# Performance work log

Hardware: AMD Instinct MI355X
Metric: run time of the kernel (lower is better)

The kernel has to match this reference:

```python
import jax, jax.numpy as jnp
import numpy as np

BERT_DIM = 768
N_ROWS = 5
N_COLS = 12
LN_EPS = 1e-5


def setup_inputs() -> dict:
    key = jax.random.key(0)
    ks = jax.random.split(key, 12)
    B, S = 256, 512
    token_hidden = jax.random.normal(ks[0], (B, S, BERT_DIM), dtype=jnp.float32)
    attention_mask = jax.random.randint(ks[1], (B, S), 0, 2, dtype=jnp.int32)
    s = lambda fan_in: 1.0 / np.sqrt(fan_in)
    return {
        "token_hidden": token_hidden,
        "attention_mask": attention_mask,
        # token_attention: Linear(768,128) -> Tanh -> Linear(128,1)
        "att_w1": jax.random.normal(ks[2], (128, BERT_DIM), dtype=jnp.float32) * s(BERT_DIM),
        "att_b1": jnp.zeros((128,), dtype=jnp.float32),
        "att_w2": jax.random.normal(ks[3], (1, 128), dtype=jnp.float32) * s(128),
        "att_b2": jnp.zeros((1,), dtype=jnp.float32),
        # feature_projector: Linear(768,256) -> GELU -> Dropout(eval) -> Linear(256,5)
        "proj_w1": jax.random.normal(ks[4], (256, BERT_DIM), dtype=jnp.float32) * s(BERT_DIM),
        "proj_b1": jnp.zeros((256,), dtype=jnp.float32),
        "proj_w2": jax.random.normal(ks[5], (N_ROWS, 256), dtype=jnp.float32) * s(256),
        "proj_b2": jnp.zeros((N_ROWS,), dtype=jnp.float32),
        # LayerNorm([5, 12])
        "ln_gamma": jnp.ones((N_ROWS, N_COLS), dtype=jnp.float32),
        "ln_beta": jnp.zeros((N_ROWS, N_COLS), dtype=jnp.float32),
    }


def reference(token_hidden, attention_mask, att_w1, att_b1, att_w2, att_b2,
              proj_w1, proj_b1, proj_w2, proj_b2, ln_gamma, ln_beta):
    # token attention scores: [B, S]
    h = jnp.tanh(jnp.einsum("bsd,hd->bsh", token_hidden, att_w1) + att_b1)
    scores = (jnp.einsum("bsh,oh->bso", h, att_w2) + att_b2)[..., 0]
    scores = jnp.where(attention_mask == 0, jnp.finfo(scores.dtype).min, scores)
    weights = jax.nn.softmax(scores, axis=-1)
    # top-k token selection (indices sorted ascending to preserve order)
    k = min(N_COLS, token_hidden.shape[1])
    _, top_idx = jax.lax.top_k(weights, k)  # [B, k]
    top_idx = jnp.sort(top_idx, axis=-1)
    selected = jnp.take_along_axis(token_hidden, top_idx[:, :, None], axis=1)  # [B, k, D]
    # feature projector (dropout is eval no-op)
    f = jax.nn.gelu(jnp.einsum("bkd,hd->bkh", selected, proj_w1) + proj_b1, approximate=False)
    f = jnp.einsum("bkh,rh->bkr", f, proj_w2) + proj_b2  # [B, k, n_rows]
    features = jnp.transpose(f, (0, 2, 1))  # [B, n_rows, k]
    if features.shape[-1] < N_COLS:
        features = jnp.pad(features, ((0, 0), (0, 0), (0, N_COLS - features.shape[-1])))
    # LayerNorm over trailing [n_rows, n_cols]
    mean = jnp.mean(features, axis=(-2, -1), keepdims=True)
    var = jnp.var(features, axis=(-2, -1), keepdims=True)
    return ln_gamma * (features - mean) * jax.lax.rsqrt(var + LN_EPS) + ln_beta
```

## Files before the change

### kernel.cpp

```cpp
#include <hip/hip_runtime.h>
#include <math.h>

#define B_BATCH 256
#define S_LEN   512
#define D_DIM   768
#define H_ATT   128
#define TOPK    12
#define NCAND   16
#define H_PROJ  256
#define N_ROWS  5
#define N_COLS  12

typedef __bf16 bf16x4 __attribute__((ext_vector_type(4)));
typedef __bf16 bf16x8 __attribute__((ext_vector_type(8)));
typedef float  f32x4  __attribute__((ext_vector_type(4)));

#define WS_SCORES 0
#define WS_WHI    524288
#define WS_WLO    720896
#define WS_W1Q    917504

__global__ __launch_bounds__(256) void prep_kernel(
    const float* __restrict__ w1, __bf16* __restrict__ whi,
    __bf16* __restrict__ wlo, float* __restrict__ w1q)
{
    int id = blockIdx.x * 256 + threadIdx.x;
    if (id < 98304) {
        int j    = id & 7;
        int lane = (id >> 3) & 63;
        int rest = id >> 9;
        int kt   = rest % 24;
        int nt   = rest / 24;
        int n = nt * 16 + (lane & 15);
        int k = kt * 32 + (lane >> 4) * 8 + j;
        float f = w1[n * D_DIM + k];
        __bf16 h = (__bf16)f;
        whi[id] = h;
        wlo[id] = (__bf16)(f - (float)h);
    } else {
        int e2 = id - 98304;
        int i  = e2 & 3;
        int n  = (e2 >> 2) & 127;
        int k4 = e2 >> 9;
        w1q[e2] = w1[n * D_DIM + k4 * 4 + i];
    }
}

__global__ __launch_bounds__(256, 3) void score_mfma(
    const float*  __restrict__ th,
    const __bf16* __restrict__ whi,
    const __bf16* __restrict__ wlo,
    const float*  __restrict__ b1,
    const float*  __restrict__ w2,
    float* __restrict__ scores)
{
    __shared__ __bf16 Ah[8 * 512];
    __shared__ __bf16 Al[8 * 512];
    __shared__ __bf16 Bh[8 * 512];
    __shared__ __bf16 Bl[8 * 512];

    const int tid = threadIdx.x;
    const int wv  = tid >> 6;
    const int ln  = tid & 63;
    const int mblk = blockIdx.x * 128;

    f32x4 acc[2][8];
    const f32x4 z = {0.f, 0.f, 0.f, 0.f};
#pragma unroll
    for (int i = 0; i < 2; ++i)
#pragma unroll
        for (int j = 0; j < 8; ++j) acc[i][j] = z;

    for (int kt = 0; kt < 24; ++kt) {
        float4 v[4];
#pragma unroll
        for (int i = 0; i < 4; ++i) {
            int f = tid + 256 * i;
            int row = f >> 3, q = f & 7;
            v[i] = *(const float4*)(th + (size_t)(mblk + row) * D_DIM + kt * 32 + q * 4);
        }
        uint4 bb[4];
#pragma unroll
        for (int i = 0; i < 4; ++i) {
            int f = tid + 256 * i;
            int r = f & 511;
            int nt = r >> 6, l = r & 63;
            const __bf16* src = (f >> 9) ? wlo : whi;
            bb[i] = *(const uint4*)(src + ((size_t)(nt * 24 + kt) * 64 + l) * 8);
        }
        __syncthreads();

#pragma unroll
        for (int i = 0; i < 4; ++i) {
            int f = tid + 256 * i;
            int row = f >> 3, q = f & 7;
            int mt = row >> 4, kq = q >> 1;
            int l16 = (row & 15) | (kq << 4);
            int a16 = l16 ^ (kq << 2);
            __bf16 h0 = (__bf16)v[i].x, h1 = (__bf16)v[i].y;
            __bf16 h2 = (__bf16)v[i].z, h3 = (__bf16)v[i].w;
            bf16x4 hv = {h0, h1, h2, h3};
            bf16x4 lv = {(__bf16)(v[i].x - (float)h0), (__bf16)(v[i].y - (float)h1),
                         (__bf16)(v[i].z - (float)h2), (__bf16)(v[i].w - (float)h3)};
            int off = mt * 512 + a16 * 8 + (q & 1) * 4;
            *(bf16x4*)(&Ah[off]) = hv;
            *(bf16x4*)(&Al[off]) = lv;
        }
#pragma unroll
        for (int i = 0; i < 4; ++i) {
            int f = tid + 256 * i;
            int r = f & 511;
            int nt = r >> 6, l = r & 63;
            __bf16* dst = (f >> 9) ? Bl : Bh;
            *(uint4*)(&dst[nt * 512 + l * 8]) = bb[i];
        }
        __syncthreads();

        const int al = ln ^ (((ln >> 4) & 3) << 2);
        bf16x8 ah0 = *(bf16x8*)(&Ah[(wv * 2 + 0) * 512 + al * 8]);
        bf16x8 ah1 = *(bf16x8*)(&Ah[(wv * 2 + 1) * 512 + al * 8]);
        bf16x8 al0 = *(bf16x8*)(&Al[(wv * 2 + 0) * 512 + al * 8]);
        bf16x8 al1 = *(bf16x8*)(&Al[(wv * 2 + 1) * 512 + al * 8]);
#pragma unroll
        for (int nt = 0; nt < 8; ++nt) {
            bf16x8 bh = *(bf16x8*)(&Bh[nt * 512 + ln * 8]);
            bf16x8 bl = *(bf16x8*)(&Bl[nt * 512 + ln * 8]);
            acc[0][nt] = __builtin_amdgcn_mfma_f32_16x16x32_bf16(ah0, bh, acc[0][nt], 0, 0, 0);
            acc[0][nt] = __builtin_amdgcn_mfma_f32_16x16x32_bf16(ah0, bl, acc[0][nt], 0, 0, 0);
            acc[0][nt] = __builtin_amdgcn_mfma_f32_16x16x32_bf16(al0, bh, acc[0][nt], 0, 0, 0);
            acc[1][nt] = __builtin_amdgcn_mfma_f32_16x16x32_bf16(ah1, bh, acc[1][nt], 0, 0, 0);
            acc[1][nt] = __builtin_amdgcn_mfma_f32_16x16x32_bf16(ah1, bl, acc[1][nt], 0, 0, 0);
            acc[1][nt] = __builtin_amdgcn_mfma_f32_16x16x32_bf16(al1, bh, acc[1][nt], 0, 0, 0);
        }
    }

    const int col = ln & 15;
    float b1v[8], w2v[8];
#pragma unroll
    for (int nt = 0; nt < 8; ++nt) {
        b1v[nt] = b1[nt * 16 + col];
        w2v[nt] = w2[nt * 16 + col];
    }
#pragma unroll
    for (int mf = 0; mf < 2; ++mf)
#pragma unroll
        for (int r = 0; r < 4; ++r) {
            float s = 0.f;
#pragma unroll
            for (int nt = 0; nt < 8; ++nt)
                s += tanhf(acc[mf][nt][r] + b1v[nt]) * w2v[nt];
            s += __shfl_xor(s, 1, 64);
            s += __shfl_xor(s, 2, 64);
            s += __shfl_xor(s, 4, 64);
            s += __shfl_xor(s, 8, 64);
            if (col == 0)
                scores[mblk + wv * 32 + mf * 16 + (ln >> 4) * 4 + r] = s;
        }
}

__global__ __launch_bounds__(256) void select_kernel(
    const float* __restrict__ th,
    const int*   __restrict__ mask,
    const float* __restrict__ ascores,
    const float* __restrict__ w1q,
    const float* __restrict__ ab1,
    const float* __restrict__ aw2,
    const float* __restrict__ pw1,
    const float* __restrict__ pb1,
    const float* __restrict__ pw2,
    const float* __restrict__ pb2,
    const float* __restrict__ gamma,
    const float* __restrict__ beta,
    float* __restrict__ out)
{
    const int b   = blockIdx.x;
    const int tid = threadIdx.x;
    const int wv  = tid >> 6;
    const int ln  = tid & 63;

    __shared__ float4 xc[NCAND][192];
    __shared__ float sc[S_LEN];
    __shared__ unsigned long long wbest[4];
    __shared__ int   cand[NCAND];
    __shared__ float redW[4][8];
    __shared__ float exact_sc[NCAND];
    __shared__ int   sel_slot[TOPK];
    __shared__ float gbuf[TOPK][H_PROJ + 1];
    __shared__ float feat[N_ROWS * N_COLS];
    __shared__ float stats[2];

    const float NEG_MIN = -3.402823466e38f;

    for (int i = tid; i < S_LEN; i += 256) {
        float s = ascores[(size_t)b * S_LEN + i];
        sc[i] = (mask[(size_t)b * S_LEN + i] == 0) ? NEG_MIN : s;
    }
    __syncthreads();

    for (int it = 0; it < NCAND; ++it) {
        float v0 = sc[tid], v1 = sc[tid + 256];
        unsigned k0 = __float_as_uint(v0);
        k0 = ((int)k0 >= 0) ? (k0 | 0x80000000u) : ~k0;
        unsigned k1 = __float_as_uint(v1);
        k1 = ((int)k1 >= 0) ? (k1 | 0x80000000u) : ~k1;
        unsigned long long p0 = ((unsigned long long)k0 << 32) | (0xFFFFFFFFu - (unsigned)tid);
        unsigned long long p1 = ((unsigned long long)k1 << 32) | (0xFFFFFFFFu - (unsigned)(tid + 256));
        unsigned long long best = p0 > p1 ? p0 : p1;
#pragma unroll
        for (int m = 1; m <= 32; m <<= 1) {
            unsigned long long o = __shfl_xor(best, m, 64);
            if (o > best) best = o;
        }
        if (ln == 0) wbest[wv] = best;
        __syncthreads();
        if (tid == 0) {
            unsigned long long bb = wbest[0];
            for (int w = 1; w < 4; ++w) if (wbest[w] > bb) bb = wbest[w];
            int idx = (int)(0xFFFFFFFFu - (unsigned)(bb & 0xFFFFFFFFu));
            cand[it] = idx;
            sc[idx] = -INFINITY;
        }
        __syncthreads();
    }

#pragma unroll
    for (int i = 0; i < 12; ++i) {
        int f = tid + 256 * i;
        int c = f / 192, k4 = f % 192;
        xc[c][k4] = *(const float4*)(th + ((size_t)b * S_LEN + cand[c]) * D_DIM + k4 * 4);
    }
    __syncthreads();

    {
        const int n = tid & 127;
        const int h = tid >> 7;
        float accs[8];
#pragma unroll
        for (int ci = 0; ci < 8; ++ci) accs[ci] = 0.f;
        for (int k4 = 0; k4 < 192; ++k4) {
            float4 w = *(const float4*)(w1q + (size_t)(k4 * 128 + n) * 4);
#pragma unroll
            for (int ci = 0; ci < 8; ++ci) {
                float4 x = xc[2 * ci + h][k4];
                accs[ci] += w.x * x.x + w.y * x.y + w.z * x.z + w.w * x.w;
            }
        }
        float b1n = ab1[n], w2n = aw2[n];
#pragma unroll
        for (int ci = 0; ci < 8; ++ci) {
            float val = tanhf(accs[ci] + b1n) * w2n;
            val += __shfl_xor(val, 1, 64);
            val += __shfl_xor(val, 2, 64);
            val += __shfl_xor(val, 4, 64);
            val += __shfl_xor(val, 8, 64);
            val += __shfl_xor(val, 16, 64);
            val += __shfl_xor(val, 32, 64);
            if (ln == 0) redW[wv][ci] = val;
        }
    }
    __syncthreads();
    if (tid < NCAND) {
        int c = tid;
        float ex = (c & 1) ? (redW[2][c >> 1] + redW[3][c >> 1])
                           : (redW[0][c >> 1] + redW[1][c >> 1]);
        if (mask[(size_t)b * S_LEN + cand[c]] == 0) ex = -INFINITY;
        exact_sc[c] = ex;
    }
    __syncthreads();

    if (tid == 0) {
        unsigned picked = 0;
        int slots[TOPK];
        for (int it = 0; it < TOPK; ++it) {
            float best = -INFINITY; int bslot = -1; int bidx = 1 << 30;
            for (int c = 0; c < NCAND; ++c) {
                if (picked & (1u << c)) continue;
                float e = exact_sc[c]; int idx = cand[c];
                if (e > best || (e == best && idx < bidx)) { best = e; bslot = c; bidx = idx; }
            }
            picked |= 1u << bslot;
            slots[it] = bslot;
        }
        for (int i = 1; i < TOPK; ++i) {
            int s = slots[i], key = cand[s], j = i - 1;
            while (j >= 0 && cand[slots[j]] > key) { slots[j + 1] = slots[j]; --j; }
            slots[j + 1] = s;
        }
        for (int t = 0; t < TOPK; ++t) sel_slot[t] = slots[t];
    }
    __syncthreads();

    {
        const int j = tid;
        int slots[TOPK];
#pragma unroll
        for (int t = 0; t < TOPK; ++t) slots[t] = sel_slot[t];
        float accp[TOPK];
        float bj = pb1[j];
#pragma unroll
        for (int t = 0; t < TOPK; ++t) accp[t] = bj;
        const float4* wrow = (const float4*)(pw1 + (size_t)j * D_DIM);
        for (int k4 = 0; k4 < 192; ++k4) {
            float4 w = wrow[k4];
#pragma unroll
            for (int t = 0; t < TOPK; ++t) {
                float4 x = xc[slots[t]][k4];
                accp[t] += w.x * x.x + w.y * x.y + w.z * x.z + w.w * x.w;
            }
        }
#pragma unroll
        for (int t = 0; t < TOPK; ++t) {
            float hh = accp[t];
            gbuf[t][j] = 0.5f * hh * (1.0f + erff(hh * 0.70710678118654752f));
        }
    }
    __syncthreads();

    if (tid < TOPK * N_ROWS) {
        int t = tid / N_ROWS, r = tid % N_ROWS;
        float s = pb2[r];
        for (int j = 0; j < H_PROJ; ++j) s += gbuf[t][j] * pw2[r * H_PROJ + j];
        feat[r * N_COLS + t] = s;
    }
    __syncthreads();

    if (tid == 0) {
        float sum = 0.f;
        for (int i = 0; i < N_ROWS * N_COLS; ++i) sum += feat[i];
        float mean = sum / 60.f;
        float sq = 0.f;
        for (int i = 0; i < N_ROWS * N_COLS; ++i) { float d = feat[i] - mean; sq += d * d; }
        stats[0] = mean;
        stats[1] = sq / 60.f;
    }
    __syncthreads();
    if (tid < N_ROWS * N_COLS) {
        float x = feat[tid];
        out[(size_t)b * 60 + tid] =
            gamma[tid] * (x - stats[0]) * rsqrtf(stats[1] + 1e-5f) + beta[tid];
    }
}

extern "C" void kernel_launch(void* const* d_in, const int* in_sizes, int n_in,
                              void* d_out, int out_size, void* d_ws, size_t ws_size,
                              hipStream_t stream) {
    const float* th   = (const float*)d_in[0];
    const int*   mask = (const int*)  d_in[1];
    const float* aw1  = (const float*)d_in[2];
    const float* ab1  = (const float*)d_in[3];
    const float* aw2  = (const float*)d_in[4];
    const float* pw1  = (const float*)d_in[6];
    const float* pb1  = (const float*)d_in[7];
    const float* pw2  = (const float*)d_in[8];
    const float* pb2  = (const float*)d_in[9];
    const float* gam  = (const float*)d_in[10];
    const float* bet  = (const float*)d_in[11];
    float* out = (float*)d_out;

    char* ws = (char*)d_ws;
    float*  scores = (float*)(ws + WS_SCORES);
    __bf16* whi    = (__bf16*)(ws + WS_WHI);
    __bf16* wlo    = (__bf16*)(ws + WS_WLO);
    float*  w1q    = (float*)(ws + WS_W1Q);

    hipLaunchKernelGGL(prep_kernel, dim3(768), dim3(256), 0, stream,
                       aw1, whi, wlo, w1q);
    hipLaunchKernelGGL(score_mfma, dim3(131072 / 128), dim3(256), 0, stream,
                       th, whi, wlo, ab1, aw2, scores);
    hipLaunchKernelGGL(select_kernel, dim3(B_BATCH), dim3(256), 0, stream,
                       th, mask, scores, w1q, ab1, aw2,
                       pw1, pb1, pw2, pb2, gam, bet, out);
}
```

Baseline: 767.7 us.

## Drop LDS staging in score GEMM, parallelize top-k and projector layout

The score kernel no longer stages A/B tiles through shared memory with block-wide barriers. Each wave loads its own token rows directly from global memory with a one-step register prefetch, and reads pre-swizzled bf16 weight fragments straight from global/L2. The select kernel replaces the 16 sequential block-wide argmax rounds with per-wave top-16 extraction followed by a single-wave merge. The projector first layer now uses a transposed copy of the weights made in the prep kernel, so each thread owns 4 hidden units × 3 tokens with coalesced weight loads. This removes barriers and LDS traffic, but relies on L2 for weight reuse across waves.

```diff
diff --git a/kernel.cpp b/kernel.cpp
--- a/kernel.cpp
+++ b/kernel.cpp
@@ -11,7 +11,6 @@
 #define N_ROWS  5
 #define N_COLS  12
 
-typedef __bf16 bf16x4 __attribute__((ext_vector_type(4)));
 typedef __bf16 bf16x8 __attribute__((ext_vector_type(8)));
 typedef float  f32x4  __attribute__((ext_vector_type(4)));
 
@@ -19,10 +18,13 @@
 #define WS_WHI    524288
 #define WS_WLO    720896
 #define WS_W1Q    917504
+#define WS_W1P    1310720
 
 __global__ __launch_bounds__(256) void prep_kernel(
-    const float* __restrict__ w1, __bf16* __restrict__ whi,
-    __bf16* __restrict__ wlo, float* __restrict__ w1q)
+    const float* __restrict__ w1,
+    const float* __restrict__ pw1,
+    __bf16* __restrict__ whi, __bf16* __restrict__ wlo,
+    float* __restrict__ w1q, float* __restrict__ w1p)
 {
     int id = blockIdx.x * 256 + threadIdx.x;
     if (id < 98304) {
@@ -37,16 +39,32 @@
         __bf16 h = (__bf16)f;
         whi[id] = h;
         wlo[id] = (__bf16)(f - (float)h);
-    } else {
+    } else if (id < 196608) {
         int e2 = id - 98304;
         int i  = e2 & 3;
         int n  = (e2 >> 2) & 127;
         int k4 = e2 >> 9;
         w1q[e2] = w1[n * D_DIM + k4 * 4 + i];
-    }
-}
-
-__global__ __launch_bounds__(256, 3) void score_mfma(
+    } else {
+        int e  = id - 196608;
+        int i  = e & 3;
+        int j  = (e >> 2) & 255;
+        int k4 = e >> 10;
+        w1p[e] = pw1[j * D_DIM + k4 * 4 + i];
+    }
+}
+
+__device__ inline void split8(float4 a, float4 b, bf16x8& hi, bf16x8& lo) {
+    float v[8] = {a.x, a.y, a.z, a.w, b.x, b.y, b.z, b.w};
+#pragma unroll
+    for (int i = 0; i < 8; ++i) {
+        __bf16 h = (__bf16)v[i];
+        hi[i] = h;
+        lo[i] = (__bf16)(v[i] - (float)h);
+    }
+}
+
+__global__ __launch_bounds__(256) void score_mfma(
     const float*  __restrict__ th,
     const __bf16* __restrict__ whi,
     const __bf16* __restrict__ wlo,
@@ -54,15 +72,12 @@
     const float*  __restrict__ w2,
     float* __restrict__ scores)
 {
-    __shared__ __bf16 Ah[8 * 512];
-    __shared__ __bf16 Al[8 * 512];
-    __shared__ __bf16 Bh[8 * 512];
-    __shared__ __bf16 Bl[8 * 512];
-
-    const int tid = threadIdx.x;
-    const int wv  = tid >> 6;
-    const int ln  = tid & 63;
-    const int mblk = blockIdx.x * 128;
+    const int ln = threadIdx.x & 63;
+    const int gw = (blockIdx.x * 256 + threadIdx.x) >> 6;
+
+    const size_t row0 = (size_t)gw * 32 + (ln & 15);
+    const float* pa0 = th + row0 * D_DIM + (ln >> 4) * 8;
+    const float* pa1 = pa0 + 16 * D_DIM;
 
     f32x4 acc[2][8];
     const f32x4 z = {0.f, 0.f, 0.f, 0.f};
@@ -71,67 +86,36 @@
 #pragma unroll
         for (int j = 0; j < 8; ++j) acc[i][j] = z;
 
+    float4 c00 = *(const float4*)(pa0);
+    float4 c01 = *(const float4*)(pa0 + 4);
+    float4 c10 = *(const float4*)(pa1);
+    float4 c11 = *(const float4*)(pa1 + 4);
+
     for (int kt = 0; kt < 24; ++kt) {
-        float4 v[4];
-#pragma unroll
-        for (int i = 0; i < 4; ++i) {
-            int f = tid + 256 * i;
-            int row = f >> 3, q = f & 7;
-            v[i] = *(const float4*)(th + (size_t)(mblk + row) * D_DIM + kt * 32 + q * 4);
-        }
-        uint4 bb[4];
-#pragma unroll
-        for (int i = 0; i < 4; ++i) {
-            int f = tid + 256 * i;
-            int r = f & 511;
-            int nt = r >> 6, l = r & 63;
-            const __bf16* src = (f >> 9) ? wlo : whi;
-            bb[i] = *(const uint4*)(src + ((size_t)(nt * 24 + kt) * 64 + l) * 8);
-        }
-        __syncthreads();
-
-#pragma unroll
-        for (int i = 0; i < 4; ++i) {
-            int f = tid + 256 * i;
-            int row = f >> 3, q = f & 7;
-            int mt = row >> 4, kq = q >> 1;
-            int l16 = (row & 15) | (kq << 4);
-            int a16 = l16 ^ (kq << 2);
-            __bf16 h0 = (__bf16)v[i].x, h1 = (__bf16)v[i].y;
-            __bf16 h2 = (__bf16)v[i].z, h3 = (__bf16)v[i].w;
-            bf16x4 hv = {h0, h1, h2, h3};
-            bf16x4 lv = {(__bf16)(v[i].x - (float)h0), (__bf16)(v[i].y - (float)h1),
-                         (__bf16)(v[i].z - (float)h2), (__bf16)(v[i].w - (float)h3)};
-            int off = mt * 512 + a16 * 8 + (q & 1) * 4;
-            *(bf16x4*)(&Ah[off]) = hv;
-            *(bf16x4*)(&Al[off]) = lv;
-        }
-#pragma unroll
-        for (int i = 0; i < 4; ++i) {
-            int f = tid + 256 * i;
-            int r = f & 511;
-            int nt = r >> 6, l = r & 63;
-            __bf16* dst = (f >> 9) ? Bl : Bh;
-            *(uint4*)(&dst[nt * 512 + l * 8]) = bb[i];
-        }
-        __syncthreads();
-
-        const int al = ln ^ (((ln >> 4) & 3) << 2);
-        bf16x8 ah0 = *(bf16x8*)(&Ah[(wv * 2 + 0) * 512 + al * 8]);
-        bf16x8 ah1 = *(bf16x8*)(&Ah[(wv * 2 + 1) * 512 + al * 8]);
-        bf16x8 al0 = *(bf16x8*)(&Al[(wv * 2 + 0) * 512 + al * 8]);
-        bf16x8 al1 = *(bf16x8*)(&Al[(wv * 2 + 1) * 512 + al * 8]);
+        const int ktn = (kt < 23) ? kt + 1 : 23;
+        float4 n00 = *(const float4*)(pa0 + ktn * 32);
+        float4 n01 = *(const float4*)(pa0 + ktn * 32 + 4);
+        float4 n10 = *(const float4*)(pa1 + ktn * 32);
+        float4 n11 = *(const float4*)(pa1 + ktn * 32 + 4);
+
+        bf16x8 ah0, al0, ah1, al1;
+        split8(c00, c01, ah0, al0);
+        split8(c10, c11, ah1, al1);
+
+        const __bf16* bhp = whi + ((size_t)kt * 64 + ln) * 8;
+        const __bf16* blp = wlo + ((size_t)kt * 64 + ln) * 8;
 #pragma unroll
         for (int nt = 0; nt < 8; ++nt) {
-            bf16x8 bh = *(bf16x8*)(&Bh[nt * 512 + ln * 8]);
-            bf16x8 bl = *(bf16x8*)(&Bl[nt * 512 + ln * 8]);
+            bf16x8 bh = *(const bf16x8*)(bhp + (size_t)nt * 24 * 512);
+            bf16x8 bl = *(const bf16x8*)(blp + (size_t)nt * 24 * 512);
             acc[0][nt] = __builtin_amdgcn_mfma_f32_16x16x32_bf16(ah0, bh, acc[0][nt], 0, 0, 0);
+            acc[0][nt] = __builtin_amdgcn_mfma_f32_16x16x32_bf16(al0, bh, acc[0][nt], 0, 0, 0);
             acc[0][nt] = __builtin_amdgcn_mfma_f32_16x16x32_bf16(ah0, bl, acc[0][nt], 0, 0, 0);
-            acc[0][nt] = __builtin_amdgcn_mfma_f32_16x16x32_bf16(al0, bh, acc[0][nt], 0, 0, 0);
             acc[1][nt] = __builtin_amdgcn_mfma_f32_16x16x32_bf16(ah1, bh, acc[1][nt], 0, 0, 0);
+            acc[1][nt] = __builtin_amdgcn_mfma_f32_16x16x32_bf16(al1, bh, acc[1][nt], 0, 0, 0);
             acc[1][nt] = __builtin_amdgcn_mfma_f32_16x16x32_bf16(ah1, bl, acc[1][nt], 0, 0, 0);
-            acc[1][nt] = __builtin_amdgcn_mfma_f32_16x16x32_bf16(al1, bh, acc[1][nt], 0, 0, 0);
-        }
+        }
+        c00 = n00; c01 = n01; c10 = n10; c11 = n11;
     }
 
     const int col = ln & 15;
@@ -154,7 +138,7 @@
             s += __shfl_xor(s, 4, 64);
             s += __shfl_xor(s, 8, 64);
             if (col == 0)
-                scores[mblk + wv * 32 + mf * 16 + (ln >> 4) * 4 + r] = s;
+                scores[(size_t)gw * 32 + mf * 16 + (ln >> 4) * 4 + r] = s;
         }
 }
 
@@ -165,7 +149,7 @@
     const float* __restrict__ w1q,
     const float* __restrict__ ab1,
     const float* __restrict__ aw2,
-    const float* __restrict__ pw1,
+    const float* __restrict__ w1p,
     const float* __restrict__ pb1,
     const float* __restrict__ pw2,
     const float* __restrict__ pb2,
@@ -179,8 +163,7 @@
     const int ln  = tid & 63;
 
     __shared__ float4 xc[NCAND][192];
-    __shared__ float sc[S_LEN];
-    __shared__ unsigned long long wbest[4];
+    __shared__ unsigned long long wtop[64];
     __shared__ int   cand[NCAND];
     __shared__ float redW[4][8];
     __shared__ float exact_sc[NCAND];
@@ -191,37 +174,45 @@
 
     const float NEG_MIN = -3.402823466e38f;
 
-    for (int i = tid; i < S_LEN; i += 256) {
-        float s = ascores[(size_t)b * S_LEN + i];
-        sc[i] = (mask[(size_t)b * S_LEN + i] == 0) ? NEG_MIN : s;
-    }
-    __syncthreads();
-
-    for (int it = 0; it < NCAND; ++it) {
-        float v0 = sc[tid], v1 = sc[tid + 256];
+    {
+        int i0 = wv * 128 + ln, i1 = i0 + 64;
+        float v0 = ascores[(size_t)b * S_LEN + i0];
+        if (mask[(size_t)b * S_LEN + i0] == 0) v0 = NEG_MIN;
+        float v1 = ascores[(size_t)b * S_LEN + i1];
+        if (mask[(size_t)b * S_LEN + i1] == 0) v1 = NEG_MIN;
         unsigned k0 = __float_as_uint(v0);
         k0 = ((int)k0 >= 0) ? (k0 | 0x80000000u) : ~k0;
         unsigned k1 = __float_as_uint(v1);
         k1 = ((int)k1 >= 0) ? (k1 | 0x80000000u) : ~k1;
-        unsigned long long p0 = ((unsigned long long)k0 << 32) | (0xFFFFFFFFu - (unsigned)tid);
-        unsigned long long p1 = ((unsigned long long)k1 << 32) | (0xFFFFFFFFu - (unsigned)(tid + 256));
-        unsigned long long best = p0 > p1 ? p0 : p1;
-#pragma unroll
-        for (int m = 1; m <= 32; m <<= 1) {
-            unsigned long long o = __shfl_xor(best, m, 64);
-            if (o > best) best = o;
-        }
-        if (ln == 0) wbest[wv] = best;
-        __syncthreads();
-        if (tid == 0) {
-            unsigned long long bb = wbest[0];
-            for (int w = 1; w < 4; ++w) if (wbest[w] > bb) bb = wbest[w];
-            int idx = (int)(0xFFFFFFFFu - (unsigned)(bb & 0xFFFFFFFFu));
-            cand[it] = idx;
-            sc[idx] = -INFINITY;
-        }
-        __syncthreads();
-    }
+        unsigned long long p0 = ((unsigned long long)k0 << 32) | (0xFFFFFFFFu - (unsigned)i0);
+        unsigned long long p1 = ((unsigned long long)k1 << 32) | (0xFFFFFFFFu - (unsigned)i1);
+        for (int it = 0; it < NCAND; ++it) {
+            unsigned long long m = p0 > p1 ? p0 : p1;
+#pragma unroll
+            for (int s = 1; s <= 32; s <<= 1) {
+                unsigned long long o = __shfl_xor(m, s, 64);
+                if (o > m) m = o;
+            }
+            if (ln == 0) wtop[wv * 16 + it] = m;
+            if (p0 == m) p0 = 0ull;
+            else if (p1 == m) p1 = 0ull;
+        }
+    }
+    __syncthreads();
+    if (wv == 0) {
+        unsigned long long q = wtop[ln];
+        for (int it = 0; it < NCAND; ++it) {
+            unsigned long long m = q;
+#pragma unroll
+            for (int s = 1; s <= 32; s <<= 1) {
+                unsigned long long o = __shfl_xor(m, s, 64);
+                if (o > m) m = o;
+            }
+            if (ln == 0) cand[it] = (int)(0xFFFFFFFFu - (unsigned)(m & 0xFFFFFFFFu));
+            if (q == m) q = 0ull;
+        }
+    }
+    __syncthreads();
 
 #pragma unroll
     for (int i = 0; i < 12; ++i) {
@@ -291,28 +282,34 @@
     __syncthreads();
 
     {
-        const int j = tid;
-        int slots[TOPK];
-#pragma unroll
-        for (int t = 0; t < TOPK; ++t) slots[t] = sel_slot[t];
-        float accp[TOPK];
-        float bj = pb1[j];
-#pragma unroll
-        for (int t = 0; t < TOPK; ++t) accp[t] = bj;
-        const float4* wrow = (const float4*)(pw1 + (size_t)j * D_DIM);
+        const int c0 = wv * 3;
+        int s0 = sel_slot[c0], s1 = sel_slot[c0 + 1], s2 = sel_slot[c0 + 2];
+        float accp[4][3];
+#pragma unroll
+        for (int cc = 0; cc < 4; ++cc) {
+            float bj = pb1[cc * 64 + ln];
+            accp[cc][0] = bj; accp[cc][1] = bj; accp[cc][2] = bj;
+        }
         for (int k4 = 0; k4 < 192; ++k4) {
-            float4 w = wrow[k4];
-#pragma unroll
-            for (int t = 0; t < TOPK; ++t) {
-                float4 x = xc[slots[t]][k4];
-                accp[t] += w.x * x.x + w.y * x.y + w.z * x.z + w.w * x.w;
-            }
-        }
-#pragma unroll
-        for (int t = 0; t < TOPK; ++t) {
-            float hh = accp[t];
-            gbuf[t][j] = 0.5f * hh * (1.0f + erff(hh * 0.70710678118654752f));
-        }
+            float4 x0 = xc[s0][k4];
+            float4 x1 = xc[s1][k4];
+            float4 x2 = xc[s2][k4];
+#pragma unroll
+            for (int cc = 0; cc < 4; ++cc) {
+                float4 w = *(const float4*)(w1p + (size_t)(k4 * 256 + cc * 64 + ln) * 4);
+                accp[cc][0] += w.x * x0.x + w.y * x0.y + w.z * x0.z + w.w * x0.w;
+                accp[cc][1] += w.x * x1.x + w.y * x1.y + w.z * x1.z + w.w * x1.w;
+                accp[cc][2] += w.x * x2.x + w.y * x2.y + w.z * x2.z + w.w * x2.w;
+            }
+        }
+#pragma unroll
+        for (int cc = 0; cc < 4; ++cc)
+#pragma unroll
+            for (int c = 0; c < 3; ++c) {
+                float hh = accp[cc][c];
+                gbuf[c0 + c][cc * 64 + ln] =
+                    0.5f * hh * (1.0f + erff(hh * 0.70710678118654752f));
+            }
     }
     __syncthreads();
 
@@ -362,12 +359,13 @@
     __bf16* whi    = (__bf16*)(ws + WS_WHI);
     __bf16* wlo    = (__bf16*)(ws + WS_WLO);
     float*  w1q    = (float*)(ws + WS_W1Q);
-
-    hipLaunchKernelGGL(prep_kernel, dim3(768), dim3(256), 0, stream,
-                       aw1, whi, wlo, w1q);
-    hipLaunchKernelGGL(score_mfma, dim3(131072 / 128), dim3(256), 0, stream,
+    float*  w1p    = (float*)(ws + WS_W1P);
+
+    hipLaunchKernelGGL(prep_kernel, dim3(1536), dim3(256), 0, stream,
+                       aw1, pw1, whi, wlo, w1q, w1p);
+    hipLaunchKernelGGL(score_mfma, dim3(1024), dim3(256), 0, stream,
                        th, whi, wlo, ab1, aw2, scores);
     hipLaunchKernelGGL(select_kernel, dim3(B_BATCH), dim3(256), 0, stream,
                        th, mask, scores, w1q, ab1, aw2,
-                       pw1, pb1, pw2, pb2, gam, bet, out);
-}
+                       w1p, pb1, pw2, pb2, gam, bet, out);
+}
```

After: 792.5 us. 1.03x slower.
